# Performance work log

Hardware: AMD Instinct MI355X
Metric: run time of the kernel (lower is better)

## Reference

```python
import jax, jax.numpy as jnp
import numpy as np

NUM_NOTES = 88
ALPHA = 0.3  # smoothing_strength
EPS = 1e-8


def _init_transition_logits(n=NUM_NOTES):
    # Faithful vectorization of _init_musical_priors (conditions checked in order).
    i = np.arange(n)[:, None]
    j = np.arange(n)[None, :]
    iv = np.abs(i - j)
    logits = np.select(
        [iv == 0, iv <= 2, iv <= 5, iv == 7, iv == 12],
        [3.0, 2.0, 1.0, 1.5, 1.0],
        default=-1.0,
    ).astype(np.float32)
    return jnp.asarray(logits)


def setup_inputs() -> dict:
    key = jax.random.key(0)
    frame_logits = jax.random.normal(key, (64, 4000, NUM_NOTES), dtype=jnp.float32)
    return {"frame_logits": frame_logits, "transition_logits": _init_transition_logits()}


def reference(frame_logits, transition_logits):
    # frame_logits: (B, T, N); transition_logits: (N, N)
    trans_probs = jax.nn.softmax(transition_logits, axis=1)          # (N, N)
    cur_probs = jax.nn.softmax(frame_logits, axis=-1)                # (B, T, N)
    first = frame_logits[:, 0, :]                                    # (B, N)

    def step(prev_smoothed, cur_p):
        prev_probs = jax.nn.softmax(prev_smoothed, axis=-1)          # (B, N)
        expected_next = prev_probs @ trans_probs                     # (B, N)
        blended = ALPHA * expected_next + (1.0 - ALPHA) * cur_p
        out = jnp.log(blended + EPS)
        return out, out

    xs = jnp.swapaxes(cur_probs[:, 1:, :], 0, 1)                     # (T-1, B, N)
    _, rest = jax.lax.scan(step, first, xs)                          # (T-1, B, N)
    rest = jnp.swapaxes(rest, 0, 1)                                  # (B, T-1, N)
    return jnp.concatenate([first[:, None, :], rest], axis=1)       # (B, T, N)
```

## Files before the change

kernel.cpp:

```cpp
#include <hip/hip_runtime.h>
#include <math.h>

#define NOTES 88
#define TSTEPS 4000
#define NCHUNK 250
#define LEN 16
#define WARMD 7
#define EPSV 1e-8f
#define PSTR 100
#define OSTR 356

typedef __attribute__((ext_vector_type(8))) short short8;
typedef __attribute__((ext_vector_type(4))) float f32x4;

__device__ __forceinline__ unsigned cvt_pk_bf16(float lo, float hi) {
    unsigned r;
    asm("v_cvt_pk_bf16_f32 %0, %1, %2" : "=v"(r) : "v"(lo), "v"(hi));
    return r;
}

__device__ __forceinline__ float hsum4(float s) {
    s += __shfl_xor(s, 16);
    s += __shfl_xor(s, 32);
    return s;
}

__global__ __launch_bounds__(64) void setup_af(const float* __restrict__ T,
                                               short8* __restrict__ afw) {
    const int l = threadIdx.x;
    const int m = l & 15, hi = l >> 4;
    __shared__ float sM[96], sI[96];
    for (int r = l; r < NOTES; r += 64) {
        const float4* row = (const float4*)(T + r * NOTES);
        float4 v[22];
#pragma unroll
        for (int q = 0; q < 22; ++q) v[q] = row[q];
        float mx = -1e30f;
#pragma unroll
        for (int q = 0; q < 22; ++q)
            mx = fmaxf(mx, fmaxf(fmaxf(v[q].x, v[q].y), fmaxf(v[q].z, v[q].w)));
        float s = 0.f;
#pragma unroll
        for (int q = 0; q < 22; ++q)
            s += __expf(v[q].x - mx) + __expf(v[q].y - mx) +
                 __expf(v[q].z - mx) + __expf(v[q].w - mx);
        sM[r] = mx;
        sI[r] = 1.0f / s;
    }
    __syncthreads();
#pragma unroll
    for (int nt = 0; nt < 6; ++nt) {
        const int n = nt * 16 + m;
#pragma unroll
        for (int kt = 0; kt < 3; ++kt) {
            float v[8];
#pragma unroll
            for (int e = 0; e < 8; ++e) {
                const int k = kt * 32 + hi * 8 + e;
                float val = 0.f;
                if (k < NOTES && n < NOTES)
                    val = __expf(T[k * NOTES + n] - sM[k]) * sI[k];
                v[e] = val;
            }
            union { unsigned u[4]; short8 s8; } uu;
#pragma unroll
            for (int q = 0; q < 4; ++q) uu.u[q] = cvt_pk_bf16(v[2 * q], v[2 * q + 1]);
            afw[(nt * 3 + kt) * 64 + l] = uu.s8;
        }
    }
}

__global__ __launch_bounds__(64, 1)
void fused_scan(const float* __restrict__ f, const short8* __restrict__ afw,
                float* __restrict__ out) {
    const int l = threadIdx.x;
    const int m = l & 15, hi = l >> 4;
    const int c = (int)(blockIdx.x % NCHUNK);
    const int bg = (int)(blockIdx.x / NCHUNK);
    const int b = bg * 16 + m;

    __shared__ unsigned short pls[16 * PSTR];
    __shared__ float so[16 * OSTR];

    short8 Af[6][3];
#pragma unroll
    for (int nt = 0; nt < 6; ++nt)
#pragma unroll
        for (int kt = 0; kt < 3; ++kt)
            Af[nt][kt] = afw[(nt * 3 + kt) * 64 + l];

    const int t0 = LEN * c;
    const int tend = t0 + LEN;
    const int tfirst = (c == 0) ? 0 : t0 - WARMD;
    const int tstore = (c == 0) ? 1 : t0;

    const float* fb = f + (size_t)b * TSTEPS * NOTES;
    const bool padq = (80 + 4 * hi) >= NOTES;
    unsigned short* pbase = pls + m * PSTR;

    auto loadRow = [&](int t, float4 (&rv)[6]) {
        const float4* rp = (const float4*)(fb + (size_t)t * NOTES);
#pragma unroll
        for (int nt = 0; nt < 6; ++nt) {
            int idx = 4 * nt + hi;
            if (nt == 5 && padq) idx = 0;
            rv[nt] = rp[idx];
        }
        if (padq) { rv[5].x = -1e30f; rv[5].y = -1e30f; rv[5].z = -1e30f; rv[5].w = -1e30f; }
    };

    auto softmaxRow = [&](const float4 (&rv)[6], float4 (&cp)[6]) {
        float s = 0.f;
#pragma unroll
        for (int nt = 0; nt < 6; ++nt) {
            cp[nt].x = __expf(rv[nt].x);
            cp[nt].y = __expf(rv[nt].y);
            cp[nt].z = __expf(rv[nt].z);
            cp[nt].w = __expf(rv[nt].w);
            s += cp[nt].x + cp[nt].y + cp[nt].z + cp[nt].w;
        }
        s = hsum4(s);
        const float inv = 1.0f / s;
#pragma unroll
        for (int nt = 0; nt < 6; ++nt) {
            cp[nt].x *= inv; cp[nt].y *= inv; cp[nt].z *= inv; cp[nt].w *= inv;
        }
    };

    auto writeP = [&](const float4 (&p)[6]) {
#pragma unroll
        for (int nt = 0; nt < 6; ++nt) {
            uint2 w;
            w.x = cvt_pk_bf16(p[nt].x, p[nt].y);
            w.y = cvt_pk_bf16(p[nt].z, p[nt].w);
            *(uint2*)(pbase + 16 * nt + 4 * hi) = w;
        }
    };

    short8 Bf[3];
    auto readB = [&]() {
#pragma unroll
        for (int kt = 0; kt < 3; ++kt)
            Bf[kt] = *(const short8*)(pbase + 32 * kt + 8 * hi);
    };

    auto flushG = [&](int tg) {
        float* obase0 = out + (size_t)(bg * 16) * TSTEPS * NOTES + (size_t)tg * NOTES;
#pragma unroll 4
        for (int mm = 0; mm < 16; ++mm) {
            const f32x4 v0 = *(const f32x4*)&so[mm * OSTR + 4 * l];
            f32x4* dst = (f32x4*)(obase0 + (size_t)mm * TSTEPS * NOTES);
            __builtin_nontemporal_store(v0, dst + l);
            if (l < 24) {
                const f32x4 v1 = *(const f32x4*)&so[mm * OSTR + 256 + 4 * l];
                __builtin_nontemporal_store(v1, dst + 64 + l);
            }
        }
    };

    auto stepS = [&](const float4 (&cur)[6], int t) {
        float4 cp[6];
        softmaxRow(cur, cp);
        f32x4 acc[6];
#pragma unroll
        for (int nt = 0; nt < 6; ++nt) acc[nt] = (f32x4){0.f, 0.f, 0.f, 0.f};
#pragma unroll
        for (int kt = 0; kt < 3; ++kt) {
#pragma unroll
            for (int nt = 0; nt < 6; ++nt)
                acc[nt] = __builtin_amdgcn_mfma_f32_16x16x32_bf16(
                    Af[nt][kt], Bf[kt], acc[nt], 0, 0, 0);
        }
        float4 x[6];
#pragma unroll
        for (int nt = 0; nt < 6; ++nt) {
            x[nt].x = fmaf(0.3f, acc[nt][0], fmaf(0.7f, cp[nt].x, EPSV));
            x[nt].y = fmaf(0.3f, acc[nt][1], fmaf(0.7f, cp[nt].y, EPSV));
            x[nt].z = fmaf(0.3f, acc[nt][2], fmaf(0.7f, cp[nt].z, EPSV));
            x[nt].w = fmaf(0.3f, acc[nt][3], fmaf(0.7f, cp[nt].w, EPSV));
        }
        writeP(x);
        readB();
        if (t >= tstore) {
            const int tm = (t - t0) & 3;
            float* sb = so + m * OSTR + tm * 88;
#pragma unroll
            for (int nt = 0; nt < 6; ++nt) {
                if (nt == 5 && padq) continue;
                float4 o;
                o.x = __logf(x[nt].x);
                o.y = __logf(x[nt].y);
                o.z = __logf(x[nt].z);
                o.w = __logf(x[nt].w);
                *(float4*)(sb + 16 * nt + 4 * hi) = o;
            }
            if (tm == 3) flushG(t - 3);
        }
    };

    {
        float4 r0[6];
        loadRow(tfirst, r0);
        float4 cp[6];
        softmaxRow(r0, cp);
        if (c == 0) {
            float* sb = so + m * OSTR;
#pragma unroll
            for (int nt = 0; nt < 6; ++nt)
                if (!(nt == 5 && padq))
                    *(float4*)(sb + 16 * nt + 4 * hi) = r0[nt];
        }
        writeP(cp);
        readB();
    }

    float4 rA[6], rB[6], rC[6];
    int t = tfirst + 1;
    loadRow(t, rA);
    {
        const int tn = (t + 1 < tend) ? t + 1 : tend - 1;
        loadRow(tn, rB);
    }
    while (true) {
        {
            const int tn = (t + 2 < tend) ? t + 2 : tend - 1;
            loadRow(tn, rC);
        }
        stepS(rA, t);
        if (++t >= tend) break;
        {
            const int tn = (t + 2 < tend) ? t + 2 : tend - 1;
            loadRow(tn, rA);
        }
        stepS(rB, t);
        if (++t >= tend) break;
        {
            const int tn = (t + 2 < tend) ? t + 2 : tend - 1;
            loadRow(tn, rB);
        }
        stepS(rC, t);
        if (++t >= tend) break;
    }
}

extern "C" void kernel_launch(void* const* d_in, const int* in_sizes, int n_in,
                              void* d_out, int out_size, void* d_ws, size_t ws_size,
                              hipStream_t stream) {
    const float* f = (const float*)d_in[0];
    const float* T = (const float*)d_in[1];
    float* out = (float*)d_out;
    short8* afw = (short8*)d_ws;
    const int batch = in_sizes[0] / (TSTEPS * NOTES);
    const int blocks = (batch / 16) * NCHUNK;
    setup_af<<<1, 64, 0, stream>>>(T, afw);
    fused_scan<<<blocks, 64, 0, stream>>>(f, afw, out);
}
```

Measured before the change: 63.24 us.

## Split scan into compute and store wavefronts with double-buffered staging

```diff
diff --git a/kernel.cpp b/kernel.cpp
--- a/kernel.cpp
+++ b/kernel.cpp
@@ -8,7 +8,7 @@
 #define WARMD 7
 #define EPSV 1e-8f
 #define PSTR 100
-#define OSTR 356
+#define OSTR2 180
 
 typedef __attribute__((ext_vector_type(8))) short short8;
 typedef __attribute__((ext_vector_type(4))) float f32x4;
@@ -70,176 +70,184 @@
     }
 }
 
-__global__ __launch_bounds__(64, 1)
+__global__ __launch_bounds__(128, 1)
 void fused_scan(const float* __restrict__ f, const short8* __restrict__ afw,
                 float* __restrict__ out) {
-    const int l = threadIdx.x;
+    const int tid = threadIdx.x;
+    const int w = tid >> 6;
+    const int l = tid & 63;
     const int m = l & 15, hi = l >> 4;
     const int c = (int)(blockIdx.x % NCHUNK);
     const int bg = (int)(blockIdx.x / NCHUNK);
-    const int b = bg * 16 + m;
 
     __shared__ unsigned short pls[16 * PSTR];
-    __shared__ float so[16 * OSTR];
-
-    short8 Af[6][3];
-#pragma unroll
-    for (int nt = 0; nt < 6; ++nt)
-#pragma unroll
-        for (int kt = 0; kt < 3; ++kt)
-            Af[nt][kt] = afw[(nt * 3 + kt) * 64 + l];
+    __shared__ float stg[2][16 * OSTR2];
 
     const int t0 = LEN * c;
     const int tend = t0 + LEN;
     const int tfirst = (c == 0) ? 0 : t0 - WARMD;
     const int tstore = (c == 0) ? 1 : t0;
 
-    const float* fb = f + (size_t)b * TSTEPS * NOTES;
-    const bool padq = (80 + 4 * hi) >= NOTES;
-    unsigned short* pbase = pls + m * PSTR;
-
-    auto loadRow = [&](int t, float4 (&rv)[6]) {
-        const float4* rp = (const float4*)(fb + (size_t)t * NOTES);
-#pragma unroll
-        for (int nt = 0; nt < 6; ++nt) {
-            int idx = 4 * nt + hi;
-            if (nt == 5 && padq) idx = 0;
-            rv[nt] = rp[idx];
-        }
-        if (padq) { rv[5].x = -1e30f; rv[5].y = -1e30f; rv[5].z = -1e30f; rv[5].w = -1e30f; }
-    };
-
-    auto softmaxRow = [&](const float4 (&rv)[6], float4 (&cp)[6]) {
-        float s = 0.f;
-#pragma unroll
-        for (int nt = 0; nt < 6; ++nt) {
-            cp[nt].x = __expf(rv[nt].x);
-            cp[nt].y = __expf(rv[nt].y);
-            cp[nt].z = __expf(rv[nt].z);
-            cp[nt].w = __expf(rv[nt].w);
-            s += cp[nt].x + cp[nt].y + cp[nt].z + cp[nt].w;
-        }
-        s = hsum4(s);
-        const float inv = 1.0f / s;
-#pragma unroll
-        for (int nt = 0; nt < 6; ++nt) {
-            cp[nt].x *= inv; cp[nt].y *= inv; cp[nt].z *= inv; cp[nt].w *= inv;
-        }
-    };
-
-    auto writeP = [&](const float4 (&p)[6]) {
-#pragma unroll
-        for (int nt = 0; nt < 6; ++nt) {
-            uint2 w;
-            w.x = cvt_pk_bf16(p[nt].x, p[nt].y);
-            w.y = cvt_pk_bf16(p[nt].z, p[nt].w);
-            *(uint2*)(pbase + 16 * nt + 4 * hi) = w;
-        }
-    };
-
-    short8 Bf[3];
-    auto readB = [&]() {
-#pragma unroll
-        for (int kt = 0; kt < 3; ++kt)
-            Bf[kt] = *(const short8*)(pbase + 32 * kt + 8 * hi);
-    };
-
-    auto flushG = [&](int tg) {
-        float* obase0 = out + (size_t)(bg * 16) * TSTEPS * NOTES + (size_t)tg * NOTES;
+    if (w == 0) {
+        const int b = bg * 16 + m;
+        const float* fb = f + (size_t)b * TSTEPS * NOTES;
+        const bool padq = (80 + 4 * hi) >= NOTES;
+        unsigned short* pbase = pls + m * PSTR;
+
+        short8 Af[6][3];
+#pragma unroll
+        for (int nt = 0; nt < 6; ++nt)
+#pragma unroll
+            for (int kt = 0; kt < 3; ++kt)
+                Af[nt][kt] = afw[(nt * 3 + kt) * 64 + l];
+
+        auto loadRow = [&](int t, float4 (&rv)[6]) {
+            const float4* rp = (const float4*)(fb + (size_t)t * NOTES);
+#pragma unroll
+            for (int nt = 0; nt < 6; ++nt) {
+                int idx = 4 * nt + hi;
+                if (nt == 5 && padq) idx = 0;
+                rv[nt] = rp[idx];
+            }
+            if (padq) { rv[5].x = -1e30f; rv[5].y = -1e30f; rv[5].z = -1e30f; rv[5].w = -1e30f; }
+        };
+
+        auto softmaxRow = [&](const float4 (&rv)[6], float4 (&cp)[6]) {
+            float s = 0.f;
+#pragma unroll
+            for (int nt = 0; nt < 6; ++nt) {
+                cp[nt].x = __expf(rv[nt].x);
+                cp[nt].y = __expf(rv[nt].y);
+                cp[nt].z = __expf(rv[nt].z);
+                cp[nt].w = __expf(rv[nt].w);
+                s += cp[nt].x + cp[nt].y + cp[nt].z + cp[nt].w;
+            }
+            s = hsum4(s);
+            const float inv = 1.0f / s;
+#pragma unroll
+            for (int nt = 0; nt < 6; ++nt) {
+                cp[nt].x *= inv; cp[nt].y *= inv; cp[nt].z *= inv; cp[nt].w *= inv;
+            }
+        };
+
+        auto writeP = [&](const float4 (&p)[6]) {
+#pragma unroll
+            for (int nt = 0; nt < 6; ++nt) {
+                uint2 wv;
+                wv.x = cvt_pk_bf16(p[nt].x, p[nt].y);
+                wv.y = cvt_pk_bf16(p[nt].z, p[nt].w);
+                *(uint2*)(pbase + 16 * nt + 4 * hi) = wv;
+            }
+        };
+
+        short8 Bf[3];
+        auto readB = [&]() {
+#pragma unroll
+            for (int kt = 0; kt < 3; ++kt)
+                Bf[kt] = *(const short8*)(pbase + 32 * kt + 8 * hi);
+        };
+
+        auto stepS = [&](const float4 (&cur)[6], int t) {
+            float4 cp[6];
+            softmaxRow(cur, cp);
+            f32x4 acc[6];
+#pragma unroll
+            for (int nt = 0; nt < 6; ++nt) acc[nt] = (f32x4){0.f, 0.f, 0.f, 0.f};
+#pragma unroll
+            for (int kt = 0; kt < 3; ++kt) {
+#pragma unroll
+                for (int nt = 0; nt < 6; ++nt)
+                    acc[nt] = __builtin_amdgcn_mfma_f32_16x16x32_bf16(
+                        Af[nt][kt], Bf[kt], acc[nt], 0, 0, 0);
+            }
+            float4 x[6];
+#pragma unroll
+            for (int nt = 0; nt < 6; ++nt) {
+                x[nt].x = fmaf(0.3f, acc[nt][0], fmaf(0.7f, cp[nt].x, EPSV));
+                x[nt].y = fmaf(0.3f, acc[nt][1], fmaf(0.7f, cp[nt].y, EPSV));
+                x[nt].z = fmaf(0.3f, acc[nt][2], fmaf(0.7f, cp[nt].z, EPSV));
+                x[nt].w = fmaf(0.3f, acc[nt][3], fmaf(0.7f, cp[nt].w, EPSV));
+            }
+            writeP(x);
+            readB();
+            if (t >= tstore) {
+                const int tm = (t - t0) & 1;
+                const int gb = ((t - t0) >> 1) & 1;
+                float* sb = &stg[gb][m * OSTR2 + tm * 88];
+#pragma unroll
+                for (int nt = 0; nt < 6; ++nt) {
+                    if (nt == 5 && padq) continue;
+                    *(float4*)(sb + 16 * nt + 4 * hi) = x[nt];
+                }
+            }
+            if (t > t0 && ((t - t0) & 1)) __syncthreads();
+        };
+
+        {
+            float4 r0[6], cp[6];
+            loadRow(tfirst, r0);
+            softmaxRow(r0, cp);
+            if (c == 0) {
+                float* sb = &stg[0][m * OSTR2];
+#pragma unroll
+                for (int nt = 0; nt < 6; ++nt)
+                    if (!(nt == 5 && padq))
+                        *(float4*)(sb + 16 * nt + 4 * hi) = r0[nt];
+            }
+            writeP(cp);
+            readB();
+        }
+
+        float4 rA[6], rB[6], rC[6];
+        int t = tfirst + 1;
+        loadRow(t, rA);
+        {
+            const int tn = (t + 1 < tend) ? t + 1 : tend - 1;
+            loadRow(tn, rB);
+        }
+        while (true) {
+            {
+                const int tn = (t + 2 < tend) ? t + 2 : tend - 1;
+                loadRow(tn, rC);
+            }
+            stepS(rA, t);
+            if (++t >= tend) break;
+            {
+                const int tn = (t + 2 < tend) ? t + 2 : tend - 1;
+                loadRow(tn, rA);
+            }
+            stepS(rB, t);
+            if (++t >= tend) break;
+            {
+                const int tn = (t + 2 < tend) ? t + 2 : tend - 1;
+                loadRow(tn, rB);
+            }
+            stepS(rC, t);
+            if (++t >= tend) break;
+        }
+    } else {
+        float* ob0 = out + (size_t)(bg * 16) * TSTEPS * NOTES;
+        for (int g = 0; g < 8; ++g) {
+            __syncthreads();
+            const int tg = t0 + 2 * g;
+            const float* sb = stg[g & 1];
+            const bool nolog = (c == 0 && g == 0 && l < 22);
+            if (l < 44) {
 #pragma unroll 4
-        for (int mm = 0; mm < 16; ++mm) {
-            const f32x4 v0 = *(const f32x4*)&so[mm * OSTR + 4 * l];
-            f32x4* dst = (f32x4*)(obase0 + (size_t)mm * TSTEPS * NOTES);
-            __builtin_nontemporal_store(v0, dst + l);
-            if (l < 24) {
-                const f32x4 v1 = *(const f32x4*)&so[mm * OSTR + 256 + 4 * l];
-                __builtin_nontemporal_store(v1, dst + 64 + l);
-            }
-        }
-    };
-
-    auto stepS = [&](const float4 (&cur)[6], int t) {
-        float4 cp[6];
-        softmaxRow(cur, cp);
-        f32x4 acc[6];
-#pragma unroll
-        for (int nt = 0; nt < 6; ++nt) acc[nt] = (f32x4){0.f, 0.f, 0.f, 0.f};
-#pragma unroll
-        for (int kt = 0; kt < 3; ++kt) {
-#pragma unroll
-            for (int nt = 0; nt < 6; ++nt)
-                acc[nt] = __builtin_amdgcn_mfma_f32_16x16x32_bf16(
-                    Af[nt][kt], Bf[kt], acc[nt], 0, 0, 0);
-        }
-        float4 x[6];
-#pragma unroll
-        for (int nt = 0; nt < 6; ++nt) {
-            x[nt].x = fmaf(0.3f, acc[nt][0], fmaf(0.7f, cp[nt].x, EPSV));
-            x[nt].y = fmaf(0.3f, acc[nt][1], fmaf(0.7f, cp[nt].y, EPSV));
-            x[nt].z = fmaf(0.3f, acc[nt][2], fmaf(0.7f, cp[nt].z, EPSV));
-            x[nt].w = fmaf(0.3f, acc[nt][3], fmaf(0.7f, cp[nt].w, EPSV));
-        }
-        writeP(x);
-        readB();
-        if (t >= tstore) {
-            const int tm = (t - t0) & 3;
-            float* sb = so + m * OSTR + tm * 88;
-#pragma unroll
-            for (int nt = 0; nt < 6; ++nt) {
-                if (nt == 5 && padq) continue;
-                float4 o;
-                o.x = __logf(x[nt].x);
-                o.y = __logf(x[nt].y);
-                o.z = __logf(x[nt].z);
-                o.w = __logf(x[nt].w);
-                *(float4*)(sb + 16 * nt + 4 * hi) = o;
-            }
-            if (tm == 3) flushG(t - 3);
-        }
-    };
-
-    {
-        float4 r0[6];
-        loadRow(tfirst, r0);
-        float4 cp[6];
-        softmaxRow(r0, cp);
-        if (c == 0) {
-            float* sb = so + m * OSTR;
-#pragma unroll
-            for (int nt = 0; nt < 6; ++nt)
-                if (!(nt == 5 && padq))
-                    *(float4*)(sb + 16 * nt + 4 * hi) = r0[nt];
-        }
-        writeP(cp);
-        readB();
-    }
-
-    float4 rA[6], rB[6], rC[6];
-    int t = tfirst + 1;
-    loadRow(t, rA);
-    {
-        const int tn = (t + 1 < tend) ? t + 1 : tend - 1;
-        loadRow(tn, rB);
-    }
-    while (true) {
-        {
-            const int tn = (t + 2 < tend) ? t + 2 : tend - 1;
-            loadRow(tn, rC);
-        }
-        stepS(rA, t);
-        if (++t >= tend) break;
-        {
-            const int tn = (t + 2 < tend) ? t + 2 : tend - 1;
-            loadRow(tn, rA);
-        }
-        stepS(rB, t);
-        if (++t >= tend) break;
-        {
-            const int tn = (t + 2 < tend) ? t + 2 : tend - 1;
-            loadRow(tn, rB);
-        }
-        stepS(rC, t);
-        if (++t >= tend) break;
+                for (int mm = 0; mm < 16; ++mm) {
+                    f32x4 v = *(const f32x4*)&sb[mm * OSTR2 + 4 * l];
+                    if (!nolog) {
+                        v[0] = __logf(v[0]);
+                        v[1] = __logf(v[1]);
+                        v[2] = __logf(v[2]);
+                        v[3] = __logf(v[3]);
+                    }
+                    __builtin_nontemporal_store(
+                        v, (f32x4*)(ob0 + (size_t)mm * TSTEPS * NOTES +
+                                    (size_t)tg * NOTES) + l);
+                }
+            }
+        }
     }
 }
 
@@ -253,5 +261,5 @@
     const int batch = in_sizes[0] / (TSTEPS * NOTES);
     const int blocks = (batch / 16) * NCHUNK;
     setup_af<<<1, 64, 0, stream>>>(T, afw);
-    fused_scan<<<blocks, 64, 0, stream>>>(f, afw, out);
-}
+    fused_scan<<<blocks, 128, 0, stream>>>(f, afw, out);
+}
```

Result: faster. 61.71 us (-2.4%).
